# Performance work log

Measured on AMD Instinct MI355X. Metric: run time of the kernel, lower is better.

## Reference

```python
import jax, jax.numpy as jnp
import numpy as np

N, C, T, H, W = 2, 512, 8, 28, 28
THW = T * H * W
BN_EPS = 1e-5


def conv1x1(x, Wt, b):
    # pointwise channel mixing, equivalent to 1x1 Conv2d/Conv3d on (N,C,T,H,W)
    return jnp.einsum('oc,ncthw->nothw', Wt, x) + b[None, :, None, None, None]


def setup_inputs() -> dict:
    key = jax.random.key(0)
    ks = jax.random.split(key, 8)
    s = 1.0 / np.sqrt(C)
    x = jax.random.normal(ks[0], (N, C, T, H, W), dtype=jnp.float32)
    mask = jax.random.uniform(ks[1], (N, C, T, H, W), dtype=jnp.float32)
    Wh = jax.random.normal(ks[2], (C, C), dtype=jnp.float32) * s
    Wg = jax.random.normal(ks[3], (C, C), dtype=jnp.float32) * s
    Wm = jax.random.normal(ks[4], (C, C), dtype=jnp.float32) * s
    Wz = jax.random.normal(ks[5], (C, C), dtype=jnp.float32) * s  # kaiming-like
    bh = jnp.zeros((C,), jnp.float32)
    bg = jnp.zeros((C,), jnp.float32)
    bm = jnp.zeros((C,), jnp.float32)
    bz = jnp.zeros((C,), jnp.float32)
    bn_w = jnp.ones((C,), jnp.float32)
    bn_b = jnp.zeros((C,), jnp.float32)
    gamma = jnp.float32(1.0)  # self.gamma (undefined in source __init__); learnable scalar
    return dict(x=x, mask=mask, Wh=Wh, bh=bh, Wg=Wg, bg=bg, Wm=Wm, bm=bm,
                Wz=Wz, bz=bz, bn_w=bn_w, bn_b=bn_b, gamma=gamma)


def reference(x, mask, Wh, bh, Wg, bg, Wm, bm, Wz, bz, bn_w, bn_b, gamma):
    n = x.shape[0]
    # proj_f = h(x) reshaped (N, THW, C); proj_g = g(x) (N, C, THW)
    ph_x = conv1x1(x, Wh, bh).reshape(n, C, THW)
    pg = conv1x1(x, Wg, bg).reshape(n, C, THW)
    # energy[n,t,s] = sum_c ph_x[n,c,t] * pg[n,c,s]  -> (N, THW, THW)
    energy = jnp.einsum('nct,ncs->nts', ph_x, pg)
    attention = jax.nn.softmax(energy, axis=-1)
    # proj_h uses self.h on mask (faithful to source)
    ph_m = conv1x1(mask, Wh, bh).reshape(n, C, THW)
    # bmm(proj_h, attention^T): [n,c,t] = sum_s ph_m[n,c,s] * attention[n,t,s]
    mask_energy = jnp.einsum('ncs,nts->nct', ph_m, attention)
    mask_atten = jax.nn.softmax(mask_energy, axis=-1)  # softmax over THW
    pm = conv1x1(x, Wm, bm)
    out = pm * mask_atten.reshape(n, C, T, H, W)
    # W_z: 1x1 Conv3d + BatchNorm3d (training-mode batch stats, weight=1, bias=0)
    wy = conv1x1(x, Wz, bz)
    mu = jnp.mean(wy, axis=(0, 2, 3, 4), keepdims=True)
    var = jnp.var(wy, axis=(0, 2, 3, 4), keepdims=True)
    wy = (wy - mu) * jax.lax.rsqrt(var + BN_EPS)
    wy = wy * bn_w[None, :, None, None, None] + bn_b[None, :, None, None, None]
    return gamma * out + wy
```

## Files before the change

### kernel.cpp

```cpp
#include <hip/hip_runtime.h>
#include <hip/hip_bf16.h>
#include <math.h>

#define NN 2
#define CC 512
#define PP 6272
#define TCHMAX 1664
#define NCHK 4
#define NJT 49
#define EM 64.0f
static const size_t PPC = (size_t)PP * CC;
static const size_t NCP = (size_t)NN * PPC;

typedef unsigned short ushortT;
typedef __attribute__((ext_vector_type(8))) short short8;
typedef __attribute__((ext_vector_type(4))) float f32x4;

__device__ __forceinline__ ushortT f2bf(float f) {
  __hip_bfloat16 h = __float2bfloat16(f);
  return *reinterpret_cast<ushortT*>(&h);
}
__device__ __forceinline__ float bf2f(ushortT u) {
  return __uint_as_float(((unsigned)u) << 16);
}

__device__ __forceinline__ void ld_g2l(const void* g, void* l) {
  __builtin_amdgcn_global_load_lds(
      (const __attribute__((address_space(1))) void*)g,
      (__attribute__((address_space(3))) void*)l, 16, 0, 0);
}

__device__ __forceinline__ int xcd_remap(int orig, int nwg) {
  const int q = nwg >> 3, r = nwg & 7;
  const int x = orig & 7, lo = orig >> 3;
  return (x < r) ? x * (q + 1) + lo : r * (q + 1) + (x - r) * q + lo;
}

__global__ __launch_bounds__(256) void k_cast4(const float* __restrict__ W0,
                                               const float* __restrict__ W1,
                                               const float* __restrict__ W2,
                                               const float* __restrict__ W3,
                                               ushortT* __restrict__ dst) {
  const float* src = (blockIdx.y == 0) ? W0 : (blockIdx.y == 1) ? W1
                    : (blockIdx.y == 2) ? W2 : W3;
  const int i = (blockIdx.x * 256 + threadIdx.x) * 4;
  float4 v = *(const float4*)&src[i];
  ushort4 o;
  o.x = f2bf(v.x); o.y = f2bf(v.y); o.z = f2bf(v.z); o.w = f2bf(v.w);
  *(ushort4*)&dst[(size_t)blockIdx.y * CC * CC + i] = o;
}

__global__ void k_castT2(const float* __restrict__ x,
                         const float* __restrict__ mask,
                         ushortT* __restrict__ xT,
                         ushortT* __restrict__ maskT) {
  __shared__ float T[32][33];
  const int zz = blockIdx.z;
  const float* in = (zz < 2) ? x : mask;
  ushortT* out = (zz < 2) ? xT : maskT;
  const int p0 = blockIdx.x * 32, c0 = blockIdx.y * 32;
  const int tx = threadIdx.x, ty = threadIdx.y;
  const size_t nbi = (size_t)(zz & 1) * PPC;
#pragma unroll
  for (int i = 0; i < 4; ++i)
    T[ty + i * 8][tx] = in[nbi + (size_t)(c0 + ty + i * 8) * PP + p0 + tx];
  __syncthreads();
#pragma unroll
  for (int i = 0; i < 4; ++i) {
    int r = ty + i * 8;
    out[nbi + (size_t)(p0 + r) * CC + c0 + tx] = f2bf(T[tx][r]);
  }
}

__global__ __launch_bounds__(256) void k_convs(
    const ushortT* __restrict__ xT, const ushortT* __restrict__ maskT,
    const ushortT* __restrict__ Whbf, const ushortT* __restrict__ Wgbf,
    const ushortT* __restrict__ Wmbf, const ushortT* __restrict__ Wzbf,
    const float* __restrict__ bh, const float* __restrict__ bg,
    const float* __restrict__ bm, const float* __restrict__ bz,
    ushortT* __restrict__ phxT, ushortT* __restrict__ pgT,
    ushortT* __restrict__ phmB, ushortT* __restrict__ pmB,
    ushortT* __restrict__ wzb) {
  __shared__ __align__(16) ushortT smem[24576];
  ushortT* S0 = smem;
  ushortT* S1 = smem + 8192;
  ushortT* S2 = smem + 16384;
  const int tid = threadIdx.x;
  const int l = tid & 63, w = tid >> 6;
  const int orig = blockIdx.x;
  const int wgid = (orig & 7) * 147 + (orig >> 3);
  const int zq = wgid / 196;
  const int within = wgid % 196;
  const int ctile = within & 3;
  const int ptile = within >> 2;
  const int wA = (w & 1) * 64, wB = (w >> 1) * 64;
  const int lr = l & 15, lk = l >> 4;
  const int sr = l >> 3, scg = l & 7;
  const int r4 = (l >> 4) * 4;

  auto stage = [&](const ushortT* src, int baseRow, ushortT* dst, int k0) {
#pragma unroll
    for (int i = 0; i < 4; ++i) {
      int row = w * 32 + i * 8 + sr;
      int cs = scg ^ (row & 7);
      ld_g2l(src + (size_t)(baseRow + row) * CC + k0 + cs * 8,
             (char*)dst + (w * 4 + i) * 1024);
    }
  };
  auto ldf = [&](const ushortT* base, int rbase, int cc_, short8* f) {
#pragma unroll
    for (int t = 0; t < 4; ++t) {
      int row = rbase + t * 16 + lr;
      f[t] = *(const short8*)((const char*)base + row * 128 +
                              ((cc_ ^ (row & 7)) * 16));
    }
  };

  if (zq < 2) {
    const int zb = zq;
    const ushortT* A = xT + (size_t)zb * PPC;
    ushortT* o1 = phxT + (size_t)zb * PPC;
    ushortT* o2 = pgT + (size_t)zb * PPC;
    const int p0 = ptile * 128, c0 = ctile * 128;
    f32x4 a1[4][4] = {}, a2[4][4] = {};
    for (int k0 = 0; k0 < CC; k0 += 64) {
      stage(A, p0, S0, k0);
      stage(Whbf, c0, S1, k0);
      stage(Wgbf, c0, S2, k0);
      __syncthreads();
#pragma unroll
      for (int ks = 0; ks < 2; ++ks) {
        short8 fp[4], f1[4], f2[4];
        const int cc = ks * 4 + lk;
        ldf(S0, wA, cc, fp);
        ldf(S1, wB, cc, f1);
        ldf(S2, wB, cc, f2);
#pragma unroll
        for (int ss = 0; ss < 4; ++ss)
#pragma unroll
          for (int tt = 0; tt < 4; ++tt) {
            a1[ss][tt] = __builtin_amdgcn_mfma_f32_16x16x32_bf16(f1[ss], fp[tt], a1[ss][tt], 0, 0, 0);
            a2[ss][tt] = __builtin_amdgcn_mfma_f32_16x16x32_bf16(f2[ss], fp[tt], a2[ss][tt], 0, 0, 0);
          }
      }
      __syncthreads();
    }
#pragma unroll
    for (int tt = 0; tt < 4; ++tt) {
      const size_t prow = (size_t)(p0 + wA + tt * 16 + lr) * CC;
#pragma unroll
      for (int ss = 0; ss < 4; ++ss) {
        const int co = c0 + wB + ss * 16 + r4;
        float4 b1v = *(const float4*)&bh[co];
        float4 b2v = *(const float4*)&bg[co];
        ushort4 v1, v2;
        v1.x = f2bf(a1[ss][tt][0] + b1v.x);
        v1.y = f2bf(a1[ss][tt][1] + b1v.y);
        v1.z = f2bf(a1[ss][tt][2] + b1v.z);
        v1.w = f2bf(a1[ss][tt][3] + b1v.w);
        v2.x = f2bf(a2[ss][tt][0] + b2v.x);
        v2.y = f2bf(a2[ss][tt][1] + b2v.y);
        v2.z = f2bf(a2[ss][tt][2] + b2v.z);
        v2.w = f2bf(a2[ss][tt][3] + b2v.w);
        *(ushort4*)&o1[prow + co] = v1;
        *(ushort4*)&o2[prow + co] = v2;
      }
    }
  } else if (zq < 4) {
    const int zb = zq - 2;
    const ushortT* B = maskT + (size_t)zb * PPC;
    ushortT* o = phmB + (size_t)zb * PPC;
    const int s0 = ptile * 128, c0 = ctile * 128;
    f32x4 a[4][4] = {};
    for (int k0 = 0; k0 < CC; k0 += 64) {
      stage(Whbf, c0, S0, k0);
      stage(B, s0, S1, k0);
      __syncthreads();
#pragma unroll
      for (int ks = 0; ks < 2; ++ks) {
        short8 fs[4], fc[4];
        const int cc = ks * 4 + lk;
        ldf(S1, wA, cc, fs);
        ldf(S0, wB, cc, fc);
#pragma unroll
        for (int ss = 0; ss < 4; ++ss)
#pragma unroll
          for (int tt = 0; tt < 4; ++tt)
            a[ss][tt] = __builtin_amdgcn_mfma_f32_16x16x32_bf16(fs[ss], fc[tt], a[ss][tt], 0, 0, 0);
      }
      __syncthreads();
    }
#pragma unroll
    for (int tt = 0; tt < 4; ++tt) {
      const int c = c0 + wB + tt * 16 + lr;
      const float bi = bh[c];
      const size_t crow = (size_t)c * PP;
#pragma unroll
      for (int ss = 0; ss < 4; ++ss) {
        ushort4 v;
        v.x = f2bf(a[ss][tt][0] + bi);
        v.y = f2bf(a[ss][tt][1] + bi);
        v.z = f2bf(a[ss][tt][2] + bi);
        v.w = f2bf(a[ss][tt][3] + bi);
        *(ushort4*)&o[crow + s0 + wA + ss * 16 + r4] = v;
      }
    }
  } else {
    const int zb = zq - 4;
    const ushortT* B = xT + (size_t)zb * PPC;
    ushortT* o1 = pmB + (size_t)zb * PPC;
    ushortT* o2 = wzb + (size_t)zb * PPC;
    const int p0 = ptile * 128, c0 = ctile * 128;
    f32x4 a1[4][4] = {}, a2[4][4] = {};
    for (int k0 = 0; k0 < CC; k0 += 64) {
      stage(Wmbf, c0, S0, k0);
      stage(Wzbf, c0, S1, k0);
      stage(B, p0, S2, k0);
      __syncthreads();
#pragma unroll
      for (int ks = 0; ks < 2; ++ks) {
        short8 fx[4], fm[4], fz[4];
        const int cc = ks * 4 + lk;
        ldf(S2, wA, cc, fx);
        ldf(S0, wB, cc, fm);
        ldf(S1, wB, cc, fz);
#pragma unroll
        for (int ss = 0; ss < 4; ++ss)
#pragma unroll
          for (int tt = 0; tt < 4; ++tt) {
            a1[ss][tt] = __builtin_amdgcn_mfma_f32_16x16x32_bf16(fx[ss], fm[tt], a1[ss][tt], 0, 0, 0);
            a2[ss][tt] = __builtin_amdgcn_mfma_f32_16x16x32_bf16(fx[ss], fz[tt], a2[ss][tt], 0, 0, 0);
          }
      }
      __syncthreads();
    }
#pragma unroll
    for (int tt = 0; tt < 4; ++tt) {
      const int c = c0 + wB + tt * 16 + lr;
      const float b1v = bm[c], b2v = bz[c];
      const size_t crow = (size_t)c * PP;
#pragma unroll
      for (int ss = 0; ss < 4; ++ss) {
        const size_t off = crow + p0 + wA + ss * 16 + r4;
        ushort4 v1, v2;
        v1.x = f2bf(a1[ss][tt][0] + b1v);
        v1.y = f2bf(a1[ss][tt][1] + b1v);
        v1.z = f2bf(a1[ss][tt][2] + b1v);
        v1.w = f2bf(a1[ss][tt][3] + b1v);
        v2.x = f2bf(a2[ss][tt][0] + b2v);
        v2.y = f2bf(a2[ss][tt][1] + b2v);
        v2.z = f2bf(a2[ss][tt][2] + b2v);
        v2.w = f2bf(a2[ss][tt][3] + b2v);
        *(ushort4*)&o1[off] = v1;
        *(ushort4*)&o2[off] = v2;
      }
    }
  }
}

__global__ __launch_bounds__(256) void k_energy(const ushortT* __restrict__ phxT,
                                                const ushortT* __restrict__ pgT,
                                                ushortT* __restrict__ Ech,
                                                float* __restrict__ Estat,
                                                int tbase) {
  __shared__ __align__(16) ushortT smem[16384];
  __shared__ float Ss[128][2];
  ushortT* At = smem;
  ushortT* Bt = smem + 8192;
  const int tid = threadIdx.x;
  const int l = tid & 63, w = tid >> 6;
  const int tiles = gridDim.y;
  const int orig = blockIdx.x + NJT * (blockIdx.y + tiles * blockIdx.z);
  const int wgid = xcd_remap(orig, NJT * tiles * NN);
  const int it = wgid % tiles;
  const int jt = (wgid / tiles) % NJT;
  const int z = wgid / (tiles * NJT);
  const int j0 = jt * 128;
  const int i0 = it * 128;
  const ushortT* A = phxT + (size_t)z * PPC + (size_t)tbase * CC;
  const ushortT* B = pgT + (size_t)z * PPC;
  ushortT* out = Ech + (size_t)z * TCHMAX * PP;
  const int wi = (w & 1) * 64, wj = (w >> 1) * 64;
  const int lr = l & 15, lk = l >> 4;
  const int sr = l >> 3, scg = l & 7;
  const int r4 = (l >> 4) * 4;

  f32x4 acc[4][4] = {};

  for (int k0 = 0; k0 < CC; k0 += 64) {
#pragma unroll
    for (int i = 0; i < 4; ++i) {
      int row = w * 32 + i * 8 + sr;
      int cs = scg ^ (row & 7);
      ld_g2l(A + (size_t)(i0 + row) * CC + k0 + cs * 8, (char*)At + (w * 4 + i) * 1024);
      ld_g2l(B + (size_t)(j0 + row) * CC + k0 + cs * 8, (char*)Bt + (w * 4 + i) * 1024);
    }
    __syncthreads();
#pragma unroll
    for (int ks = 0; ks < 2; ++ks) {
      short8 af[4], bfv[4];
      const int cc = ks * 4 + lk;
#pragma unroll
      for (int tt = 0; tt < 4; ++tt) {
        int row = wi + tt * 16 + lr;
        af[tt] = *(const short8*)((const char*)At + row * 128 + ((cc ^ (row & 7)) * 16));
      }
#pragma unroll
      for (int ss = 0; ss < 4; ++ss) {
        int row = wj + ss * 16 + lr;
        bfv[ss] = *(const short8*)((const char*)Bt + row * 128 + ((cc ^ (row & 7)) * 16));
      }
#pragma unroll
      for (int ss = 0; ss < 4; ++ss)
#pragma unroll
        for (int tt = 0; tt < 4; ++tt)
          acc[ss][tt] = __builtin_amdgcn_mfma_f32_16x16x32_bf16(bfv[ss], af[tt], acc[ss][tt], 0, 0, 0);
    }
    __syncthreads();
  }
#pragma unroll
  for (int tt = 0; tt < 4; ++tt) {
    const int trow = i0 + wi + tt * 16 + lr;
    ushortT* orow = out + (size_t)trow * PP + j0;
    float sx = 0.f;
#pragma unroll
    for (int ss = 0; ss < 4; ++ss) {
      float u0 = __expf(acc[ss][tt][0] - EM);
      float u1 = __expf(acc[ss][tt][1] - EM);
      float u2 = __expf(acc[ss][tt][2] - EM);
      float u3 = __expf(acc[ss][tt][3] - EM);
      sx += (u0 + u1) + (u2 + u3);
      ushort4 v;
      v.x = f2bf(u0); v.y = f2bf(u1); v.z = f2bf(u2); v.w = f2bf(u3);
      *(ushort4*)&orow[wj + ss * 16 + r4] = v;
    }
    sx += __shfl_xor(sx, 16);
    sx += __shfl_xor(sx, 32);
    if (l < 16) Ss[wi + tt * 16 + l][w >> 1] = sx;
  }
  __syncthreads();
  if (tid < 128) {
    Estat[((size_t)z * TCHMAX + i0 + tid) * NJT + jt] = Ss[tid][0] + Ss[tid][1];
  }
}

__global__ __launch_bounds__(256) void k_zcomb(const float* __restrict__ Estat,
                                               float* __restrict__ rowZ, int rows) {
  const int r = blockIdx.x * 256 + threadIdx.x;
  if (r >= NN * rows) return;
  const int z = r / rows, tl = r % rows;
  const float* p = Estat + ((size_t)z * TCHMAX + tl) * NJT;
  float s = 0.f;
#pragma unroll
  for (int j = 0; j < NJT; ++j) s += p[j];
  rowZ[z * TCHMAX + tl] = 1.0f / s;
}

template <int KSPT>
__global__ __launch_bounds__(256) void k_me(const ushortT* __restrict__ phmB,
                                            const ushortT* __restrict__ Ech,
                                            ushortT* __restrict__ mePart) {
  __shared__ __align__(16) ushortT smem[12288];
  ushortT* At = smem;
  ushortT* Bt = smem + 8192;
  const int tid = threadIdx.x;
  const int l = tid & 63, w = tid >> 6;
  const int gx = gridDim.x;
  const int orig = blockIdx.x + gx * (blockIdx.y + 4 * blockIdx.z);
  const int nwg = gx * 4 * (NN * KSPT);
  const int wgid = (orig & 7) * (nwg >> 3) + (orig >> 3);
  const int cb = wgid & 3;
  const int tl = (wgid >> 2) % gx;
  const int bz = (wgid >> 2) / gx;
  const int tl0 = tl * 64;
  const int c0 = cb * 128;
  const int z = bz / KSPT, ks = bz % KSPT;
  const size_t nb = (size_t)z * PPC;
  const ushortT* Pb = Ech + (size_t)z * TCHMAX * PP;
  const int wc = (w & 1) * 64, wt = (w >> 1) * 32;
  const int lr = l & 15, lk = l >> 4;
  const int sr = l >> 3, scg = l & 7;
  const int r4 = (l >> 4) * 4;

  f32x4 acc[2][4] = {};

  const int sBeg = ((ks * 98) / KSPT) * 64;
  const int sEnd = (((ks + 1) * 98) / KSPT) * 64;
  for (int s0 = sBeg; s0 < sEnd; s0 += 64) {
#pragma unroll
    for (int i = 0; i < 4; ++i) {
      int row = w * 32 + i * 8 + sr;
      int cs = scg ^ (row & 7);
      ld_g2l(phmB + nb + (size_t)(c0 + row) * PP + s0 + cs * 8,
             (char*)At + (w * 4 + i) * 1024);
    }
#pragma unroll
    for (int i = 0; i < 2; ++i) {
      int row = w * 16 + i * 8 + sr;
      int cs = scg ^ (row & 7);
      ld_g2l(Pb + (size_t)(tl0 + row) * PP + s0 + cs * 8,
             (char*)Bt + (w * 2 + i) * 1024);
    }
    __syncthreads();
#pragma unroll
    for (int kk = 0; kk < 2; ++kk) {
      short8 af[4], bfv[2];
      const int cc = kk * 4 + lk;
#pragma unroll
      for (int ct = 0; ct < 4; ++ct) {
        int row = wc + ct * 16 + lr;
        af[ct] = *(const short8*)((const char*)At + row * 128 + ((cc ^ (row & 7)) * 16));
      }
#pragma unroll
      for (int tt = 0; tt < 2; ++tt) {
        int row = wt + tt * 16 + lr;
        bfv[tt] = *(const short8*)((const char*)Bt + row * 128 + ((cc ^ (row & 7)) * 16));
      }
#pragma unroll
      for (int tt = 0; tt < 2; ++tt)
#pragma unroll
        for (int ct = 0; ct < 4; ++ct)
          acc[tt][ct] = __builtin_amdgcn_mfma_f32_16x16x32_bf16(bfv[tt], af[ct], acc[tt][ct], 0, 0, 0);
    }
    __syncthreads();
  }
  ushortT* out = mePart + ((size_t)(ks * NN + z) * CC) * TCHMAX;
#pragma unroll
  for (int ct = 0; ct < 4; ++ct) {
    const size_t crow = (size_t)(c0 + wc + ct * 16 + lr) * TCHMAX + tl0;
#pragma unroll
    for (int tt = 0; tt < 2; ++tt) {
      ushort4 v;
      v.x = f2bf(acc[tt][ct][0]);
      v.y = f2bf(acc[tt][ct][1]);
      v.z = f2bf(acc[tt][ct][2]);
      v.w = f2bf(acc[tt][ct][3]);
      *(ushort4*)&out[crow + wt + tt * 16 + r4] = v;
    }
  }
}

template <int KSPT>
__global__ __launch_bounds__(256) void k_meadd(const ushortT* __restrict__ mePart,
                                               const float* __restrict__ rowZ,
                                               ushortT* __restrict__ meb,
                                               int tbase, int rows) {
  const int idx = (blockIdx.x * 256 + threadIdx.x) * 4;
  const int tl = idx % rows;
  const int c = (idx / rows) % CC;
  const int z = idx / (rows * CC);
  float s0 = 0.f, s1 = 0.f, s2 = 0.f, s3 = 0.f;
#pragma unroll
  for (int ks = 0; ks < KSPT; ++ks) {
    const size_t o = ((size_t)(ks * NN + z) * CC + c) * TCHMAX + tl;
    ushort4 a = *(const ushort4*)&mePart[o];
    s0 += bf2f(a.x); s1 += bf2f(a.y); s2 += bf2f(a.z); s3 += bf2f(a.w);
  }
  const float4 rz = *(const float4*)&rowZ[z * TCHMAX + tl];
  ushort4 v;
  v.x = f2bf(s0 * rz.x); v.y = f2bf(s1 * rz.y);
  v.z = f2bf(s2 * rz.z); v.w = f2bf(s3 * rz.w);
  *(ushort4*)&meb[((size_t)z * CC + c) * PP + tbase + tl] = v;
}

__global__ __launch_bounds__(256) void k_soft2(const ushortT* __restrict__ me,
                                               float* __restrict__ m2,
                                               float* __restrict__ Z2) {
  __shared__ float red[256];
  const ushortT* row = me + (size_t)blockIdx.x * PP;
  const int tid = threadIdx.x;
  const int NCH = PP / 8;
  float m = -INFINITY;
  for (int i = tid; i < NCH; i += 256) {
    short8 v = *(const short8*)&row[i * 8];
#pragma unroll
    for (int j = 0; j < 8; ++j) m = fmaxf(m, bf2f((ushortT)v[j]));
  }
  red[tid] = m;
  __syncthreads();
  for (int s = 128; s > 0; s >>= 1) {
    if (tid < s) red[tid] = fmaxf(red[tid], red[tid + s]);
    __syncthreads();
  }
  m = red[0];
  __syncthreads();
  float zz = 0.f;
  for (int i = tid; i < NCH; i += 256) {
    short8 v = *(const short8*)&row[i * 8];
#pragma unroll
    for (int j = 0; j < 8; ++j) zz += __expf(bf2f((ushortT)v[j]) - m);
  }
  red[tid] = zz;
  __syncthreads();
  for (int s = 128; s > 0; s >>= 1) {
    if (tid < s) red[tid] += red[tid + s];
    __syncthreads();
  }
  if (tid == 0) { m2[blockIdx.x] = m; Z2[blockIdx.x] = red[0]; }
}

__global__ __launch_bounds__(256) void k_bnstat(const ushortT* __restrict__ wz,
                                                float* __restrict__ mu,
                                                float* __restrict__ rinv) {
  __shared__ float rs[256];
  __shared__ float rq[256];
  const int c = blockIdx.x;
  const int tid = threadIdx.x;
  const int NCH = PP / 8;
  float s = 0.f, q = 0.f;
  for (int n = 0; n < NN; ++n) {
    const ushortT* rowp = wz + (size_t)n * CC * PP + (size_t)c * PP;
    for (int i = tid; i < NCH; i += 256) {
      short8 v = *(const short8*)&rowp[i * 8];
#pragma unroll
      for (int j = 0; j < 8; ++j) {
        float f = bf2f((ushortT)v[j]);
        s += f;
        q += f * f;
      }
    }
  }
  rs[tid] = s; rq[tid] = q;
  __syncthreads();
  for (int st = 128; st > 0; st >>= 1) {
    if (tid < st) { rs[tid] += rs[tid + st]; rq[tid] += rq[tid + st]; }
    __syncthreads();
  }
  if (tid == 0) {
    const float inv_n = 1.0f / (float)(NN * PP);
    float mean = rs[0] * inv_n;
    float var = rq[0] * inv_n - mean * mean;
    mu[c] = mean;
    rinv[c] = rsqrtf(var + 1e-5f);
  }
}

__global__ __launch_bounds__(256) void k_final(const ushortT* __restrict__ pmB,
                                               const ushortT* __restrict__ me,
                                               const ushortT* __restrict__ wz,
                                               const float* __restrict__ m2,
                                               const float* __restrict__ Z2,
                                               const float* __restrict__ mu,
                                               const float* __restrict__ rinv,
                                               const float* __restrict__ bnw,
                                               const float* __restrict__ bnb,
                                               const float* __restrict__ gamma,
                                               float* __restrict__ out) {
  const int e4 = blockIdx.x * 256 + threadIdx.x;
  const size_t e = (size_t)e4 * 4;
  const int nc = (int)(e / PP);
  const int c = nc & (CC - 1);
  const float m = m2[nc];
  const float rz = 1.0f / Z2[nc];
  const float mub = mu[c];
  const float ri = rinv[c] * bnw[c];
  const float bb = bnb[c];
  const float g = gamma[0];
  ushort4 pv = *(const ushort4*)&pmB[e];
  ushort4 mev = *(const ushort4*)&me[e];
  ushort4 wzv = *(const ushort4*)&wz[e];
  float4 o;
  o.x = g * bf2f(pv.x) * (__expf(bf2f(mev.x) - m) * rz) + (bf2f(wzv.x) - mub) * ri + bb;
  o.y = g * bf2f(pv.y) * (__expf(bf2f(mev.y) - m) * rz) + (bf2f(wzv.y) - mub) * ri + bb;
  o.z = g * bf2f(pv.z) * (__expf(bf2f(mev.z) - m) * rz) + (bf2f(wzv.z) - mub) * ri + bb;
  o.w = g * bf2f(pv.w) * (__expf(bf2f(mev.w) - m) * rz) + (bf2f(wzv.w) - mub) * ri + bb;
  *(float4*)&out[e] = o;
}

extern "C" void kernel_launch(void* const* d_in, const int* in_sizes, int n_in,
                              void* d_out, int out_size, void* d_ws, size_t ws_size,
                              hipStream_t stream) {
  (void)in_sizes; (void)n_in; (void)out_size;
  const float* x    = (const float*)d_in[0];
  const float* mask = (const float*)d_in[1];
  const float* Wh   = (const float*)d_in[2];
  const float* bh   = (const float*)d_in[3];
  const float* Wg   = (const float*)d_in[4];
  const float* bg   = (const float*)d_in[5];
  const float* Wm   = (const float*)d_in[6];
  const float* bm   = (const float*)d_in[7];
  const float* Wz   = (const float*)d_in[8];
  const float* bz   = (const float*)d_in[9];
  const float* bnw  = (const float*)d_in[10];
  const float* bnb  = (const float*)d_in[11];
  const float* gam  = (const float*)d_in[12];

  ushortT* wzb  = (ushortT*)d_ws;
  ushortT* meb  = wzb + NCP;
  ushortT* pmB  = meb + NCP;
  ushortT* phxT = pmB + NCP;
  ushortT* pgT  = phxT + NCP;
  ushortT* phmB = pgT + NCP;
  ushortT* Wbf  = phmB + NCP;
  ushortT* Whbf = Wbf;
  ushortT* Wgbf = Wbf + 1 * CC * CC;
  ushortT* Wmbf = Wbf + 2 * CC * CC;
  ushortT* Wzbf = Wbf + 3 * CC * CC;
  float* m2    = (float*)(Wbf + 4 * CC * CC);
  float* Z2    = m2 + NN * CC;
  float* mu    = Z2 + NN * CC;
  float* rin   = mu + CC;
  float* Estat = rin + CC;
  float* rowZ  = Estat + (size_t)NN * TCHMAX * NJT;
  float* region = rowZ + (size_t)NN * TCHMAX + 16;
  ushortT* xT    = (ushortT*)region;
  ushortT* maskT = xT + NCP;
  ushortT* Ech    = (ushortT*)region;
  ushortT* mePart = Ech + (size_t)NN * TCHMAX * PP;

  const size_t regionOffB = (size_t)((char*)region - (char*)d_ws);
  const size_t need8 = regionOffB +
      ((size_t)NN * TCHMAX * PP + 8ull * NN * CC * TCHMAX) * 2;
  const bool k8 = ws_size >= need8;

  k_cast4<<<dim3(256, 4), 256, 0, stream>>>(Wh, Wg, Wm, Wz, Wbf);
  k_castT2<<<dim3(PP / 32, CC / 32, 4), dim3(32, 8), 0, stream>>>(x, mask, xT, maskT);

  k_convs<<<1176, 256, 0, stream>>>(xT, maskT, Whbf, Wgbf, Wmbf, Wzbf,
                                    bh, bg, bm, bz, phxT, pgT, phmB, pmB, wzb);

  static const int chunkTiles[NCHK] = {13, 12, 12, 12};
  int tbase = 0;
  for (int ch = 0; ch < NCHK; ++ch) {
    const int tiles = chunkTiles[ch];
    const int rows = tiles * 128;
    dim3 gE(NJT, tiles, NN);
    k_energy<<<gE, 256, 0, stream>>>(phxT, pgT, Ech, Estat, tbase);
    k_zcomb<<<(NN * rows + 255) / 256, 256, 0, stream>>>(Estat, rowZ, rows);
    if (k8) {
      dim3 gM(rows / 64, CC / 128, NN * 8);
      k_me<8><<<gM, 256, 0, stream>>>(phmB, Ech, mePart);
      k_meadd<8><<<NN * CC * rows / 1024, 256, 0, stream>>>(mePart, rowZ, meb,
                                                            tbase, rows);
    } else {
      dim3 gM(rows / 64, CC / 128, NN * 4);
      k_me<4><<<gM, 256, 0, stream>>>(phmB, Ech, mePart);
      k_meadd<4><<<NN * CC * rows / 1024, 256, 0, stream>>>(mePart, rowZ, meb,
                                                            tbase, rows);
    }
    tbase += rows;
  }

  k_soft2<<<NN * CC, 256, 0, stream>>>(meb, m2, Z2);
  k_bnstat<<<CC, 256, 0, stream>>>(wzb, mu, rin);
  const int total4 = (int)(NCP / 4);
  k_final<<<total4 / 256, 256, 0, stream>>>(pmB, meb, wzb, m2, Z2, mu, rin,
                                            bnw, bnb, gam, (float*)d_out);
}
```

Before: 561.2 us.

## Double-buffer LDS with K=32 stages in conv, energy and mask-energy GEMMs

Converts the three main bf16 MFMA GEMM kernels from single-buffered 64-wide K tiles with two barriers per step to double-buffered 32-wide K tiles, so the next tile's global-to-LDS loads are in flight while the current tile is computed, with one barrier per step. The LDS swizzle is redone for 64-byte rows and fragment offsets are precomputed outside the loop. Launch-bounds occupancy hints (3, 4, 6 blocks per CU) are added. The price is twice as many loop iterations and barriers per unit of K, plus possible register pressure from the occupancy hints.

```diff
diff --git a/kernel.cpp b/kernel.cpp
--- a/kernel.cpp
+++ b/kernel.cpp
@@ -35,6 +35,7 @@
   const int x = orig & 7, lo = orig >> 3;
   return (x < r) ? x * (q + 1) + lo : r * (q + 1) + (x - r) * q + lo;
 }
+
 
 __global__ __launch_bounds__(256) void k_cast4(const float* __restrict__ W0,
                                                const float* __restrict__ W1,
@@ -72,7 +73,7 @@
   }
 }
 
-__global__ __launch_bounds__(256) void k_convs(
+__global__ __launch_bounds__(256, 3) void k_convs(
     const ushortT* __restrict__ xT, const ushortT* __restrict__ maskT,
     const ushortT* __restrict__ Whbf, const ushortT* __restrict__ Wgbf,
     const ushortT* __restrict__ Wmbf, const ushortT* __restrict__ Wzbf,
@@ -82,9 +83,6 @@
     ushortT* __restrict__ phmB, ushortT* __restrict__ pmB,
     ushortT* __restrict__ wzb) {
   __shared__ __align__(16) ushortT smem[24576];
-  ushortT* S0 = smem;
-  ushortT* S1 = smem + 8192;
-  ushortT* S2 = smem + 16384;
   const int tid = threadIdx.x;
   const int l = tid & 63, w = tid >> 6;
   const int orig = blockIdx.x;
@@ -95,55 +93,70 @@
   const int ptile = within >> 2;
   const int wA = (w & 1) * 64, wB = (w >> 1) * 64;
   const int lr = l & 15, lk = l >> 4;
-  const int sr = l >> 3, scg = l & 7;
   const int r4 = (l >> 4) * 4;
-
-  auto stage = [&](const ushortT* src, int baseRow, ushortT* dst, int k0) {
-#pragma unroll
-    for (int i = 0; i < 4; ++i) {
-      int row = w * 32 + i * 8 + sr;
-      int cs = scg ^ (row & 7);
-      ld_g2l(src + (size_t)(baseRow + row) * CC + k0 + cs * 8,
-             (char*)dst + (w * 4 + i) * 1024);
-    }
+  const int srow = l >> 2;
+  const int sg8 = ((l & 3) ^ ((l >> 3) & 3)) * 8;
+  const int rg16 = (lk ^ ((lr >> 1) & 3)) * 16;
+
+  int offL[4], offR[4];
+#pragma unroll
+  for (int t = 0; t < 4; ++t) {
+    offL[t] = (wA + t * 16 + lr) * 64 + rg16;
+    offR[t] = (wB + t * 16 + lr) * 64 + rg16;
+  }
+
+  auto stage = [&](const ushortT* src ,
+                   ushortT* dst) {
+#pragma unroll
+    for (int i = 0; i < 2; ++i)
+      ld_g2l(src + (size_t)(w * 32 + i * 16 + srow) * CC + sg8,
+             (char*)dst + (w * 2 + i) * 1024);
   };
-  auto ldf = [&](const ushortT* base, int rbase, int cc_, short8* f) {
-#pragma unroll
-    for (int t = 0; t < 4; ++t) {
-      int row = rbase + t * 16 + lr;
-      f[t] = *(const short8*)((const char*)base + row * 128 +
-                              ((cc_ ^ (row & 7)) * 16));
-    }
+  auto ldf = [&](const ushortT* base, const int* off, short8* f) {
+#pragma unroll
+    for (int t = 0; t < 4; ++t)
+      f[t] = *(const short8*)((const char*)base + off[t]);
   };
+
+  ushortT* M0c = smem;          ushortT* M0n = smem + 4096;
+  ushortT* M1c = smem + 8192;   ushortT* M1n = smem + 12288;
+  ushortT* M2c = smem + 16384;  ushortT* M2n = smem + 20480;
 
   if (zq < 2) {
     const int zb = zq;
-    const ushortT* A = xT + (size_t)zb * PPC;
+    const int p0 = ptile * 128, c0 = ctile * 128;
+    const ushortT* Ax = xT + (size_t)zb * PPC + (size_t)p0 * CC;
+    const ushortT* Bw1 = Whbf + (size_t)c0 * CC;
+    const ushortT* Bw2 = Wgbf + (size_t)c0 * CC;
     ushortT* o1 = phxT + (size_t)zb * PPC;
     ushortT* o2 = pgT + (size_t)zb * PPC;
-    const int p0 = ptile * 128, c0 = ctile * 128;
     f32x4 a1[4][4] = {}, a2[4][4] = {};
-    for (int k0 = 0; k0 < CC; k0 += 64) {
-      stage(A, p0, S0, k0);
-      stage(Whbf, c0, S1, k0);
-      stage(Wgbf, c0, S2, k0);
+    stage(Ax, M0c); stage(Bw1, M1c); stage(Bw2, M2c);
+    __syncthreads();
+    for (int t = 0; t < 16; ++t) {
+      if (t < 15) {
+        const int k = (t + 1) * 32;
+        stage(Ax + k, M0n); stage(Bw1 + k, M1n); stage(Bw2 + k, M2n);
+      }
+      short8 fp[4], fw[4];
+      ldf(M0c, offL, fp);
+      ldf(M1c, offR, fw);
+#pragma unroll
+      for (int ss = 0; ss < 4; ++ss)
+#pragma unroll
+        for (int tt = 0; tt < 4; ++tt)
+          a1[ss][tt] = __builtin_amdgcn_mfma_f32_16x16x32_bf16(fw[ss], fp[tt], a1[ss][tt], 0, 0, 0);
+      ldf(M2c, offR, fw);
+#pragma unroll
+      for (int ss = 0; ss < 4; ++ss)
+#pragma unroll
+        for (int tt = 0; tt < 4; ++tt)
+          a2[ss][tt] = __builtin_amdgcn_mfma_f32_16x16x32_bf16(fw[ss], fp[tt], a2[ss][tt], 0, 0, 0);
       __syncthreads();
-#pragma unroll
-      for (int ks = 0; ks < 2; ++ks) {
-        short8 fp[4], f1[4], f2[4];
-        const int cc = ks * 4 + lk;
-        ldf(S0, wA, cc, fp);
-        ldf(S1, wB, cc, f1);
-        ldf(S2, wB, cc, f2);
-#pragma unroll
-        for (int ss = 0; ss < 4; ++ss)
-#pragma unroll
-          for (int tt = 0; tt < 4; ++tt) {
-            a1[ss][tt] = __builtin_amdgcn_mfma_f32_16x16x32_bf16(f1[ss], fp[tt], a1[ss][tt], 0, 0, 0);
-            a2[ss][tt] = __builtin_amdgcn_mfma_f32_16x16x32_bf16(f2[ss], fp[tt], a2[ss][tt], 0, 0, 0);
-          }
-      }
-      __syncthreads();
+      ushortT* tp;
+      tp = M0c; M0c = M0n; M0n = tp;
+      tp = M1c; M1c = M1n; M1n = tp;
+      tp = M2c; M2c = M2n; M2n = tp;
     }
 #pragma unroll
     for (int tt = 0; tt < 4; ++tt) {
@@ -168,27 +181,30 @@
     }
   } else if (zq < 4) {
     const int zb = zq - 2;
-    const ushortT* B = maskT + (size_t)zb * PPC;
+    const int s0 = ptile * 128, c0 = ctile * 128;
+    const ushortT* Am = maskT + (size_t)zb * PPC + (size_t)s0 * CC;
+    const ushortT* Bw = Whbf + (size_t)c0 * CC;
     ushortT* o = phmB + (size_t)zb * PPC;
-    const int s0 = ptile * 128, c0 = ctile * 128;
     f32x4 a[4][4] = {};
-    for (int k0 = 0; k0 < CC; k0 += 64) {
-      stage(Whbf, c0, S0, k0);
-      stage(B, s0, S1, k0);
+    stage(Am, M0c); stage(Bw, M1c);
+    __syncthreads();
+    for (int t = 0; t < 16; ++t) {
+      if (t < 15) {
+        const int k = (t + 1) * 32;
+        stage(Am + k, M0n); stage(Bw + k, M1n);
+      }
+      short8 fs[4], fc[4];
+      ldf(M0c, offL, fs);
+      ldf(M1c, offR, fc);
+#pragma unroll
+      for (int ss = 0; ss < 4; ++ss)
+#pragma unroll
+        for (int tt = 0; tt < 4; ++tt)
+          a[ss][tt] = __builtin_amdgcn_mfma_f32_16x16x32_bf16(fs[ss], fc[tt], a[ss][tt], 0, 0, 0);
       __syncthreads();
-#pragma unroll
-      for (int ks = 0; ks < 2; ++ks) {
-        short8 fs[4], fc[4];
-        const int cc = ks * 4 + lk;
-        ldf(S1, wA, cc, fs);
-        ldf(S0, wB, cc, fc);
-#pragma unroll
-        for (int ss = 0; ss < 4; ++ss)
-#pragma unroll
-          for (int tt = 0; tt < 4; ++tt)
-            a[ss][tt] = __builtin_amdgcn_mfma_f32_16x16x32_bf16(fs[ss], fc[tt], a[ss][tt], 0, 0, 0);
-      }
-      __syncthreads();
+      ushortT* tp;
+      tp = M0c; M0c = M0n; M0n = tp;
+      tp = M1c; M1c = M1n; M1n = tp;
     }
 #pragma unroll
     for (int tt = 0; tt < 4; ++tt) {
@@ -207,32 +223,39 @@
     }
   } else {
     const int zb = zq - 4;
-    const ushortT* B = xT + (size_t)zb * PPC;
+    const int p0 = ptile * 128, c0 = ctile * 128;
+    const ushortT* Ax = xT + (size_t)zb * PPC + (size_t)p0 * CC;
+    const ushortT* Bw1 = Wmbf + (size_t)c0 * CC;
+    const ushortT* Bw2 = Wzbf + (size_t)c0 * CC;
     ushortT* o1 = pmB + (size_t)zb * PPC;
     ushortT* o2 = wzb + (size_t)zb * PPC;
-    const int p0 = ptile * 128, c0 = ctile * 128;
     f32x4 a1[4][4] = {}, a2[4][4] = {};
-    for (int k0 = 0; k0 < CC; k0 += 64) {
-      stage(Wmbf, c0, S0, k0);
-      stage(Wzbf, c0, S1, k0);
-      stage(B, p0, S2, k0);
+    stage(Ax, M0c); stage(Bw1, M1c); stage(Bw2, M2c);
+    __syncthreads();
+    for (int t = 0; t < 16; ++t) {
+      if (t < 15) {
+        const int k = (t + 1) * 32;
+        stage(Ax + k, M0n); stage(Bw1 + k, M1n); stage(Bw2 + k, M2n);
+      }
+      short8 fx[4], fw[4];
+      ldf(M0c, offL, fx);
+      ldf(M1c, offR, fw);
+#pragma unroll
+      for (int ss = 0; ss < 4; ++ss)
+#pragma unroll
+        for (int tt = 0; tt < 4; ++tt)
+          a1[ss][tt] = __builtin_amdgcn_mfma_f32_16x16x32_bf16(fx[ss], fw[tt], a1[ss][tt], 0, 0, 0);
+      ldf(M2c, offR, fw);
+#pragma unroll
+      for (int ss = 0; ss < 4; ++ss)
+#pragma unroll
+        for (int tt = 0; tt < 4; ++tt)
+          a2[ss][tt] = __builtin_amdgcn_mfma_f32_16x16x32_bf16(fx[ss], fw[tt], a2[ss][tt], 0, 0, 0);
       __syncthreads();
-#pragma unroll
-      for (int ks = 0; ks < 2; ++ks) {
-        short8 fx[4], fm[4], fz[4];
-        const int cc = ks * 4 + lk;
-        ldf(S2, wA, cc, fx);
-        ldf(S0, wB, cc, fm);
-        ldf(S1, wB, cc, fz);
-#pragma unroll
-        for (int ss = 0; ss < 4; ++ss)
-#pragma unroll
-          for (int tt = 0; tt < 4; ++tt) {
-            a1[ss][tt] = __builtin_amdgcn_mfma_f32_16x16x32_bf16(fx[ss], fm[tt], a1[ss][tt], 0, 0, 0);
-            a2[ss][tt] = __builtin_amdgcn_mfma_f32_16x16x32_bf16(fx[ss], fz[tt], a2[ss][tt], 0, 0, 0);
-          }
-      }
-      __syncthreads();
+      ushortT* tp;
+      tp = M0c; M0c = M0n; M0n = tp;
+      tp = M1c; M1c = M1n; M1n = tp;
+      tp = M2c; M2c = M2n; M2n = tp;
     }
 #pragma unroll
     for (int tt = 0; tt < 4; ++tt) {
@@ -258,15 +281,13 @@
   }
 }
 
-__global__ __launch_bounds__(256) void k_energy(const ushortT* __restrict__ phxT,
-                                                const ushortT* __restrict__ pgT,
-                                                ushortT* __restrict__ Ech,
-                                                float* __restrict__ Estat,
-                                                int tbase) {
+__global__ __launch_bounds__(256, 4) void k_energy(const ushortT* __restrict__ phxT,
+                                                   const ushortT* __restrict__ pgT,
+                                                   ushortT* __restrict__ Ech,
+                                                   float* __restrict__ Estat,
+                                                   int tbase) {
   __shared__ __align__(16) ushortT smem[16384];
   __shared__ float Ss[128][2];
-  ushortT* At = smem;
-  ushortT* Bt = smem + 8192;
   const int tid = threadIdx.x;
   const int l = tid & 63, w = tid >> 6;
   const int tiles = gridDim.y;
@@ -277,46 +298,58 @@
   const int z = wgid / (tiles * NJT);
   const int j0 = jt * 128;
   const int i0 = it * 128;
-  const ushortT* A = phxT + (size_t)z * PPC + (size_t)tbase * CC;
-  const ushortT* B = pgT + (size_t)z * PPC;
+  const ushortT* Arow = phxT + (size_t)z * PPC + (size_t)(tbase + i0) * CC;
+  const ushortT* Brow = pgT + (size_t)z * PPC + (size_t)j0 * CC;
   ushortT* out = Ech + (size_t)z * TCHMAX * PP;
   const int wi = (w & 1) * 64, wj = (w >> 1) * 64;
   const int lr = l & 15, lk = l >> 4;
-  const int sr = l >> 3, scg = l & 7;
   const int r4 = (l >> 4) * 4;
+  const int srow = l >> 2;
+  const int sg8 = ((l & 3) ^ ((l >> 3) & 3)) * 8;
+  const int rg16 = (lk ^ ((lr >> 1) & 3)) * 16;
+
+  int offA[4], offB[4];
+#pragma unroll
+  for (int t = 0; t < 4; ++t) {
+    offA[t] = (wi + t * 16 + lr) * 64 + rg16;
+    offB[t] = (wj + t * 16 + lr) * 64 + rg16;
+  }
+  auto stage = [&](const ushortT* src, ushortT* dst) {
+#pragma unroll
+    for (int i = 0; i < 2; ++i)
+      ld_g2l(src + (size_t)(w * 32 + i * 16 + srow) * CC + sg8,
+             (char*)dst + (w * 2 + i) * 1024);
+  };
+
+  ushortT* A0 = smem;          ushortT* A1 = smem + 4096;
+  ushortT* B0 = smem + 8192;   ushortT* B1 = smem + 12288;
 
   f32x4 acc[4][4] = {};
 
-  for (int k0 = 0; k0 < CC; k0 += 64) {
-#pragma unroll
-    for (int i = 0; i < 4; ++i) {
-      int row = w * 32 + i * 8 + sr;
-      int cs = scg ^ (row & 7);
-      ld_g2l(A + (size_t)(i0 + row) * CC + k0 + cs * 8, (char*)At + (w * 4 + i) * 1024);
-      ld_g2l(B + (size_t)(j0 + row) * CC + k0 + cs * 8, (char*)Bt + (w * 4 + i) * 1024);
-    }
-    __syncthreads();
-#pragma unroll
-    for (int ks = 0; ks < 2; ++ks) {
-      short8 af[4], bfv[4];
-      const int cc = ks * 4 + lk;
-#pragma unroll
-      for (int tt = 0; tt < 4; ++tt) {
-        int row = wi + tt * 16 + lr;
-        af[tt] = *(const short8*)((const char*)At + row * 128 + ((cc ^ (row & 7)) * 16));
-      }
-#pragma unroll
-      for (int ss = 0; ss < 4; ++ss) {
-        int row = wj + ss * 16 + lr;
-        bfv[ss] = *(const short8*)((const char*)Bt + row * 128 + ((cc ^ (row & 7)) * 16));
-      }
-#pragma unroll
-      for (int ss = 0; ss < 4; ++ss)
-#pragma unroll
-        for (int tt = 0; tt < 4; ++tt)
-          acc[ss][tt] = __builtin_amdgcn_mfma_f32_16x16x32_bf16(bfv[ss], af[tt], acc[ss][tt], 0, 0, 0);
-    }
-    __syncthreads();
+  stage(Arow, A0); stage(Brow, B0);
+  __syncthreads();
+  ushortT *Ac = A0, *An = A1, *Bc = B0, *Bn = B1;
+  for (int t = 0; t < 16; ++t) {
+    if (t < 15) {
+      const int k = (t + 1) * 32;
+      stage(Arow + k, An); stage(Brow + k, Bn);
+    }
+    short8 af[4], bfv[4];
+#pragma unroll
+    for (int tt = 0; tt < 4; ++tt)
+      af[tt] = *(const short8*)((const char*)Ac + offA[tt]);
+#pragma unroll
+    for (int ss = 0; ss < 4; ++ss)
+      bfv[ss] = *(const short8*)((const char*)Bc + offB[ss]);
+#pragma unroll
+    for (int ss = 0; ss < 4; ++ss)
+#pragma unroll
+      for (int tt = 0; tt < 4; ++tt)
+        acc[ss][tt] = __builtin_amdgcn_mfma_f32_16x16x32_bf16(bfv[ss], af[tt], acc[ss][tt], 0, 0, 0);
+    __syncthreads();
+    ushortT* tp;
+    tp = Ac; Ac = An; An = tp;
+    tp = Bc; Bc = Bn; Bn = tp;
   }
 #pragma unroll
   for (int tt = 0; tt < 4; ++tt) {
@@ -357,12 +390,10 @@
 }
 
 template <int KSPT>
-__global__ __launch_bounds__(256) void k_me(const ushortT* __restrict__ phmB,
-                                            const ushortT* __restrict__ Ech,
-                                            ushortT* __restrict__ mePart) {
+__global__ __launch_bounds__(256, 6) void k_me(const ushortT* __restrict__ phmB,
+                                               const ushortT* __restrict__ Ech,
+                                               ushortT* __restrict__ mePart) {
   __shared__ __align__(16) ushortT smem[12288];
-  ushortT* At = smem;
-  ushortT* Bt = smem + 8192;
   const int tid = threadIdx.x;
   const int l = tid & 63, w = tid >> 6;
   const int gx = gridDim.x;
@@ -375,54 +406,64 @@
   const int tl0 = tl * 64;
   const int c0 = cb * 128;
   const int z = bz / KSPT, ks = bz % KSPT;
-  const size_t nb = (size_t)z * PPC;
-  const ushortT* Pb = Ech + (size_t)z * TCHMAX * PP;
+  const ushortT* Arow = phmB + (size_t)z * PPC + (size_t)c0 * PP;
+  const ushortT* Brow = Ech + (size_t)z * TCHMAX * PP + (size_t)tl0 * PP;
   const int wc = (w & 1) * 64, wt = (w >> 1) * 32;
   const int lr = l & 15, lk = l >> 4;
-  const int sr = l >> 3, scg = l & 7;
   const int r4 = (l >> 4) * 4;
+  const int srow = l >> 2;
+  const int sg8 = ((l & 3) ^ ((l >> 3) & 3)) * 8;
+  const int rg16 = (lk ^ ((lr >> 1) & 3)) * 16;
+
+  int offA[4], offB[2];
+#pragma unroll
+  for (int t = 0; t < 4; ++t) offA[t] = (wc + t * 16 + lr) * 64 + rg16;
+#pragma unroll
+  for (int t = 0; t < 2; ++t) offB[t] = (wt + t * 16 + lr) * 64 + rg16;
+
+  auto stA = [&](const ushortT* src, ushortT* dst) {
+#pragma unroll
+    for (int i = 0; i < 2; ++i)
+      ld_g2l(src + (size_t)(w * 32 + i * 16 + srow) * PP + sg8,
+             (char*)dst + (w * 2 + i) * 1024);
+  };
+  auto stB = [&](const ushortT* src, ushortT* dst) {
+    ld_g2l(src + (size_t)(w * 16 + srow) * PP + sg8, (char*)dst + w * 1024);
+  };
+
+  ushortT* A0 = smem;          ushortT* A1 = smem + 4096;
+  ushortT* B0 = smem + 8192;   ushortT* B1 = smem + 10240;
 
   f32x4 acc[2][4] = {};
 
   const int sBeg = ((ks * 98) / KSPT) * 64;
   const int sEnd = (((ks + 1) * 98) / KSPT) * 64;
-  for (int s0 = sBeg; s0 < sEnd; s0 += 64) {
-#pragma unroll
-    for (int i = 0; i < 4; ++i) {
-      int row = w * 32 + i * 8 + sr;
-      int cs = scg ^ (row & 7);
-      ld_g2l(phmB + nb + (size_t)(c0 + row) * PP + s0 + cs * 8,
-             (char*)At + (w * 4 + i) * 1024);
-    }
-#pragma unroll
-    for (int i = 0; i < 2; ++i) {
-      int row = w * 16 + i * 8 + sr;
-      int cs = scg ^ (row & 7);
-      ld_g2l(Pb + (size_t)(tl0 + row) * PP + s0 + cs * 8,
-             (char*)Bt + (w * 2 + i) * 1024);
-    }
-    __syncthreads();
-#pragma unroll
-    for (int kk = 0; kk < 2; ++kk) {
-      short8 af[4], bfv[2];
-      const int cc = kk * 4 + lk;
-#pragma unroll
-      for (int ct = 0; ct < 4; ++ct) {
-        int row = wc + ct * 16 + lr;
-        af[ct] = *(const short8*)((const char*)At + row * 128 + ((cc ^ (row & 7)) * 16));
-      }
-#pragma unroll
-      for (int tt = 0; tt < 2; ++tt) {
-        int row = wt + tt * 16 + lr;
-        bfv[tt] = *(const short8*)((const char*)Bt + row * 128 + ((cc ^ (row & 7)) * 16));
-      }
-#pragma unroll
-      for (int tt = 0; tt < 2; ++tt)
-#pragma unroll
-        for (int ct = 0; ct < 4; ++ct)
-          acc[tt][ct] = __builtin_amdgcn_mfma_f32_16x16x32_bf16(bfv[tt], af[ct], acc[tt][ct], 0, 0, 0);
-    }
-    __syncthreads();
+  const int NT = (sEnd - sBeg) >> 5;
+
+  stA(Arow + sBeg, A0); stB(Brow + sBeg, B0);
+  __syncthreads();
+  ushortT *Ac = A0, *An = A1, *Bc = B0, *Bn = B1;
+  for (int t = 0; t < NT; ++t) {
+    if (t + 1 < NT) {
+      const int k = sBeg + (t + 1) * 32;
+      stA(Arow + k, An); stB(Brow + k, Bn);
+    }
+    short8 af[4], bfv[2];
+#pragma unroll
+    for (int ct = 0; ct < 4; ++ct)
+      af[ct] = *(const short8*)((const char*)Ac + offA[ct]);
+#pragma unroll
+    for (int tt = 0; tt < 2; ++tt)
+      bfv[tt] = *(const short8*)((const char*)Bc + offB[tt]);
+#pragma unroll
+    for (int tt = 0; tt < 2; ++tt)
+#pragma unroll
+      for (int ct = 0; ct < 4; ++ct)
+        acc[tt][ct] = __builtin_amdgcn_mfma_f32_16x16x32_bf16(bfv[tt], af[ct], acc[tt][ct], 0, 0, 0);
+    __syncthreads();
+    ushortT* tp;
+    tp = Ac; Ac = An; An = tp;
+    tp = Bc; Bc = Bn; Bn = tp;
   }
   ushortT* out = mePart + ((size_t)(ks * NN + z) * CC) * TCHMAX;
 #pragma unroll
```

Result: slower. 579.9 us (+3.3%).
